# Kernel tuning notes

Measured on AMD Instinct MI355X. Metric: run time of the kernel, lower is better.

The kernel has to match this reference:

```python
import jax, jax.numpy as jnp
import numpy as np

HID = 256
OUT_DIM = 3


def _nearest_idx(c, size):
    # PyTorch grid_sample nearest, align_corners=False: idx = round(((c+1)*size-1)/2) = floor((c+1)*size/2)
    return jnp.clip(jnp.floor((c + 1.0) * size * 0.5), 0, size - 1).astype(jnp.int32)


def _mlp(x, params):
    # 4 hidden ReLU layers of 256 + linear out (LIIF imnet)
    for w, b in params[:-1]:
        x = jax.nn.relu(x @ w + b)
    w, b = params[-1]
    return x @ w + b


def setup_inputs() -> dict:
    key = jax.random.key(0)
    ks = jax.random.split(key, 16)
    B, C, H, W = 2, 64, 128, 128
    Q = 65536  # 256x256 HR queries
    feat = jax.random.normal(ks[0], (B, C, H, W), dtype=jnp.float32)
    coord = jax.random.uniform(ks[1], (B, Q, 2), dtype=jnp.float32) * 2.0 - 1.0  # in [-1,1)
    cell = jnp.full((B, Q, 2), 2.0 / 256.0, dtype=jnp.float32)
    in_dim = C * 9 + 2 + 2
    dims = [in_dim, HID, HID, HID, HID, OUT_DIM]
    inp = {"feat": feat, "coord": coord, "cell": cell}
    for i in range(5):
        fan_in = dims[i]
        inp[f"w{i}"] = jax.random.normal(ks[2 + 2 * i], (dims[i], dims[i + 1]), dtype=jnp.float32) / np.sqrt(fan_in)
        inp[f"b{i}"] = jnp.zeros((dims[i + 1],), dtype=jnp.float32)
    return inp


def reference(feat, coord, cell, w0, b0, w1, b1, w2, b2, w3, b3, w4, b4):
    params = [(w0, b0), (w1, b1), (w2, b2), (w3, b3), (w4, b4)]
    B, C, H, W = feat.shape
    dt = feat.dtype
    # feat_unfold: F.unfold(feat, 3, padding=1) -> channel order c*9 + (ki*3+kj)
    p = jnp.pad(feat, ((0, 0), (0, 0), (1, 1), (1, 1)))
    feat_u = jnp.stack([p[:, :, i:i + H, j:j + W] for i in range(3) for j in range(3)], axis=2)
    feat_flat = feat_u.reshape(B, C * 9, H * W)  # [B, 576, H*W]

    rx = 1.0 / H  # 2/H/2
    ry = 1.0 / W
    eps_shift = 1e-6
    lim = 1.0 - 1e-6
    rel_cell = cell * jnp.array([H, W], dtype=dt)

    preds, areas = [], []
    for vx in (-1.0, 1.0):
        for vy in (-1.0, 1.0):
            cx = jnp.clip(coord[..., 0] + vx * rx + eps_shift, -lim, lim)
            cy = jnp.clip(coord[..., 1] + vy * ry + eps_shift, -lim, lim)
            ix = _nearest_idx(cx, H)  # coord dim 0 -> height, grid is coord.flip(-1)
            iy = _nearest_idx(cy, W)
            lin = ix * W + iy  # [B, Q]
            q_feat = jnp.take_along_axis(feat_flat, lin[:, None, :], axis=2).transpose(0, 2, 1)  # [B,Q,576]
            # feat_coord grid-center values at the gathered cell (nearest gather of make_coord)
            qx = -1.0 + (2.0 * ix.astype(dt) + 1.0) / H
            qy = -1.0 + (2.0 * iy.astype(dt) + 1.0) / W
            rel = jnp.stack([(coord[..., 0] - qx) * H, (coord[..., 1] - qy) * W], axis=-1)  # [B,Q,2]
            mlp_in = jnp.concatenate([q_feat, rel, rel_cell], axis=-1)  # [B,Q,580]
            preds.append(_mlp(mlp_in, params))  # [B,Q,3]
            areas.append(jnp.abs(rel[..., 0] * rel[..., 1]) + 1e-9)

    # local_ensemble: swap diagonal areas
    areas[0], areas[3] = areas[3], areas[0]
    areas[1], areas[2] = areas[2], areas[1]
    tot = areas[0] + areas[1] + areas[2] + areas[3]
    ret = sum(pr * (a / tot)[..., None] for pr, a in zip(preds, areas))
    return ret
```

## Files before the change

### kernel.cpp

```cpp
#include <hip/hip_runtime.h>

typedef _Float16 half_t;
typedef _Float16 half4 __attribute__((ext_vector_type(4)));
typedef _Float16 half8 __attribute__((ext_vector_type(8)));
typedef float float4v __attribute__((ext_vector_type(4)));

#define MFMA16(a, b, c) __builtin_amdgcn_mfma_f32_16x16x32_f16(a, b, c, 0, 0, 0)

__device__ __host__ __forceinline__ int sigma_p(int s) {
  return (s & 0xC3) | ((s & 0x0C) << 2) | ((s & 0x30) >> 2);
}

__global__ __launch_bounds__(256) void pack_frags(
    const float* __restrict__ w0, const float* __restrict__ w1,
    const float* __restrict__ w2, const float* __restrict__ w3,
    const float* __restrict__ w4, half_t* __restrict__ w0p,
    half_t* __restrict__ w1p, half_t* __restrict__ w2p,
    half_t* __restrict__ w3p, half_t* __restrict__ w4p,
    half_t* __restrict__ wtp) {
  const int bb = blockIdx.x;
  const int tid = threadIdx.x;
  if (bb == 42) {
#pragma unroll
    for (int e = 0; e < 16; e++) {
      const int id = e * 256 + tid;
      const int j = id & 7;
      const int lane = (id >> 3) & 63;
      const int ks = id >> 9;
      const int n = lane & 15;
      const int k = ks * 32 + ((lane >> 4) << 3) + j;
      w4p[id] = (half_t)((n < 3) ? w4[sigma_p(k) * 3 + n] : 0.0f);
    }
#pragma unroll
    for (int e = 0; e < 4; e++)
      wtp[e * 256 + tid] = (half_t)w0[576 * 256 + e * 256 + sigma_p(tid)];
    return;
  }
  __shared__ float Wt[32][260];
  const float* w;
  half_t* out;
  int nks, ks;
  int mode;
  if (bb < 18) { w = w0; out = w0p; nks = 18; ks = bb; mode = 0; }
  else if (bb < 26) { w = w1; out = w1p; nks = 8; ks = bb - 18; mode = 1; }
  else if (bb < 34) { w = w2; out = w2p; nks = 8; ks = bb - 26; mode = 1; }
  else { w = w3; out = w3p; nks = 8; ks = bb - 34; mode = 1; }
  {
    const int n4 = (tid & 63) * 4;
    const int kr = tid >> 6;
#pragma unroll
    for (int e = 0; e < 8; e++) {
      const int kp = e * 4 + kr;
      int kg = ks * 32 + kp;
      if (mode == 0) { const int w9 = kg >> 6, c = kg & 63; kg = c * 9 + w9; }
      else kg = sigma_p(kg);
      *(float4v*)&Wt[kp][n4] = *(const float4v*)(w + (size_t)kg * 256 + n4);
    }
  }
  __syncthreads();
  const int lane = tid & 63;
  const int l15 = lane & 15;
  const int kq = (lane >> 4) << 3;
#pragma unroll
  for (int e = 0; e < 4; e++) {
    const int nt = e * 4 + (tid >> 6);
    half8 hv;
#pragma unroll
    for (int j = 0; j < 8; j++) hv[j] = (half_t)Wt[kq + j][nt * 16 + l15];
    *(half8*)&out[((nt * nks + ks) * 64 + lane) * 8] = hv;
  }
}

__global__ __launch_bounds__(256, 2) void conv_l0(
    const float* __restrict__ feat, const half_t* __restrict__ w0p,
    const float* __restrict__ b0, half_t* __restrict__ Z) {
  __shared__ alignas(16) half_t Xc[2][64][40];
  const int tid = threadIdx.x;
  const int lane = tid & 63, wave = tid >> 6, quad = lane >> 4, l15 = lane & 15;
  const int blk = blockIdx.x;
  const int b = blk >> 8;
  const int h = (blk >> 1) & 127;
  const int wbase = (blk & 1) << 6;
  const float* featB = feat + b * (64 * 128 * 128);

  auto stage = [&](int ks, int buf) {
    const int w9 = ks >> 1;
    const int di = w9 / 3;
    const int dj = w9 - 3 * di;
    const int pos = tid & 63;
    const int grp = tid >> 6;
    const int y = h + di - 1;
    const int x = wbase + pos + dj - 1;
    const bool ok = ((unsigned)y < 128u) && ((unsigned)x < 128u);
    const float* base = featB + (((ks & 1) * 32 + grp * 8) << 14) + (y << 7) + x;
    half4 h0, h1;
#pragma unroll
    for (int u = 0; u < 4; u++) h0[u] = (half_t)(ok ? base[u << 14] : 0.0f);
#pragma unroll
    for (int u = 0; u < 4; u++) h1[u] = (half_t)(ok ? base[(u + 4) << 14] : 0.0f);
    *(half4*)&Xc[buf][pos][grp * 8] = h0;
    *(half4*)&Xc[buf][pos][grp * 8 + 4] = h1;
  };

  const float4v zero4 = {0.0f, 0.0f, 0.0f, 0.0f};
  float4v acc[4][4];
#pragma unroll
  for (int mt = 0; mt < 4; mt++)
#pragma unroll
    for (int jn = 0; jn < 4; jn++) acc[mt][jn] = zero4;

  half8 bcur[4], bnxt[4];
#pragma unroll
  for (int jn = 0; jn < 4; jn++)
    bcur[jn] = *(const half8*)(w0p + ((((wave * 4 + jn) * 18 + 0) * 64 + lane) << 3));
  stage(0, 0);
  __syncthreads();

#pragma unroll 1
  for (int ks = 0; ks < 18; ks++) {
    const int buf = ks & 1;
    if (ks + 1 < 18) {
      stage(ks + 1, buf ^ 1);
#pragma unroll
      for (int jn = 0; jn < 4; jn++)
        bnxt[jn] =
            *(const half8*)(w0p + ((((wave * 4 + jn) * 18 + ks + 1) * 64 + lane) << 3));
    }
    half8 a[4];
#pragma unroll
    for (int mt = 0; mt < 4; mt++)
      a[mt] = *(const half8*)(&Xc[buf][mt * 16 + l15][quad * 8]);
#pragma unroll
    for (int mt = 0; mt < 4; mt++)
#pragma unroll
      for (int jn = 0; jn < 4; jn++)
        acc[mt][jn] = MFMA16(bcur[jn], a[mt], acc[mt][jn]);
#pragma unroll
    for (int jn = 0; jn < 4; jn++) bcur[jn] = bnxt[jn];
    __syncthreads();
  }

  float4v bb[4];
#pragma unroll
  for (int jn = 0; jn < 4; jn++)
    bb[jn] = *(const float4v*)(b0 + (wave * 4 + jn) * 16 + quad * 4);
  const int posbase = b * 16384 + h * 128 + wbase;
#pragma unroll
  for (int mt = 0; mt < 4; mt++) {
    half8 o0, o1;
#pragma unroll
    for (int jn = 0; jn < 2; jn++)
#pragma unroll
      for (int rr = 0; rr < 4; rr++) {
        o0[jn * 4 + rr] = (half_t)(acc[mt][jn][rr] + bb[jn][rr]);
        o1[jn * 4 + rr] = (half_t)(acc[mt][jn + 2][rr] + bb[jn + 2][rr]);
      }
    half_t* zp = &Z[(size_t)(posbase + mt * 16 + l15) * 256 + wave * 64 + quad * 16];
    *(half8*)zp = o0;
    *(half8*)(zp + 8) = o1;
  }
}

__global__ __launch_bounds__(256, 2) void liif_main(
    const float* __restrict__ coord, const float* __restrict__ cell,
    const half_t* __restrict__ Zp, const half_t* __restrict__ wtp,
    const half_t* __restrict__ w1p, const half_t* __restrict__ w2p,
    const half_t* __restrict__ w3p, const half_t* __restrict__ w4p,
    const float* __restrict__ b1, const float* __restrict__ b2,
    const float* __restrict__ b3, const float* __restrict__ b4,
    float* __restrict__ outp) {
  __shared__ alignas(16) half_t Hs[128][264];
  __shared__ float S4[4][128][4];
  __shared__ int pos4[4][64];
  __shared__ half_t relxh[4][64], relyh[4][64];
  __shared__ half_t cellxh[64], cellyh[64];
  __shared__ float area4[4][64];
  __shared__ float oacc[64][4];

  const int tid = threadIdx.x;
  const int lane = tid & 63;
  const int wave = tid >> 6;
  const int quad = lane >> 4;
  const int l15 = lane & 15;
  const int blk = blockIdx.x;
  const int batch = blk >> 10;

  {
    const int t = tid >> 6, row = tid & 63;
    const int gq = blk * 64 + row;
    const float cx0 = coord[gq * 2 + 0], cy0 = coord[gq * 2 + 1];
    const float vx = (t & 2) ? 1.0f : -1.0f;
    const float vy = (t & 1) ? 1.0f : -1.0f;
    const float r = 1.0f / 128.0f, lim = 1.0f - 1e-6f, eps = 1e-6f;
    float cx = fminf(fmaxf(cx0 + vx * r + eps, -lim), lim);
    float cy = fminf(fmaxf(cy0 + vy * r + eps, -lim), lim);
    int ix = (int)floorf((cx + 1.0f) * 64.0f);
    ix = min(max(ix, 0), 127);
    int iy = (int)floorf((cy + 1.0f) * 64.0f);
    iy = min(max(iy, 0), 127);
    float qx = -1.0f + (2.0f * ix + 1.0f) * (1.0f / 128.0f);
    float qy = -1.0f + (2.0f * iy + 1.0f) * (1.0f / 128.0f);
    float rxv = (cx0 - qx) * 128.0f;
    float ryv = (cy0 - qy) * 128.0f;
    pos4[t][row] = (batch << 14) + (ix << 7) + iy;
    relxh[t][row] = (half_t)rxv;
    relyh[t][row] = (half_t)ryv;
    area4[t][row] = fabsf(rxv * ryv) + 1e-9f;
    if (t == 0) {
      cellxh[row] = (half_t)(cell[gq * 2 + 0] * 128.0f);
      cellyh[row] = (half_t)(cell[gq * 2 + 1] * 128.0f);
      oacc[row][0] = 0.0f;
      oacc[row][1] = 0.0f;
      oacc[row][2] = 0.0f;
    }
  }
  __syncthreads();

  const float4v zero4 = {0.0f, 0.0f, 0.0f, 0.0f};
  const half8 zero8 = {0, 0, 0, 0, 0, 0, 0, 0};
  const int c8 = tid & 31;
  const int rbase = (tid >> 5) * 16;

  const half8 wt0 = *(const half8*)(wtp + 0 * 256 + c8 * 8);
  const half8 wt1 = *(const half8*)(wtp + 1 * 256 + c8 * 8);
  const half8 wt2 = *(const half8*)(wtp + 2 * 256 + c8 * 8);
  const half8 wt3 = *(const half8*)(wtp + 3 * 256 + c8 * 8);

  half8 bcur[4], bnxt[4], bf4[2];
#pragma unroll
  for (int jn = 0; jn < 4; jn++)
    bcur[jn] = *(const half8*)(w1p + ((((wave * 4 + jn) * 8 + 0) * 64 + lane) << 3));

#pragma unroll 1
  for (int p = 0; p < 2; p++) {
#pragma unroll
    for (int e = 0; e < 16; e++) {
      const int r = rbase + e;
      const int corner = 2 * p + (r >> 6);
      const int qrow = r & 63;
      const half8 z = *(const half8*)(Zp + ((size_t)pos4[corner][qrow] << 8) + c8 * 8);
      const half_t rx = relxh[corner][qrow], ry = relyh[corner][qrow];
      const half_t cx = cellxh[qrow], cy = cellyh[qrow];
      const half8 rx8 = {rx, rx, rx, rx, rx, rx, rx, rx};
      const half8 ry8 = {ry, ry, ry, ry, ry, ry, ry, ry};
      const half8 cx8 = {cx, cx, cx, cx, cx, cx, cx, cx};
      const half8 cy8 = {cy, cy, cy, cy, cy, cy, cy, cy};
      half8 v = z + rx8 * wt0 + ry8 * wt1 + cx8 * wt2 + cy8 * wt3;
      v = __builtin_elementwise_max(v, zero8);
      *(half8*)(&Hs[r][c8 * 8]) = v;
    }
    __syncthreads();

    float4v acc[8][4];
#pragma unroll 1
    for (int L = 0; L < 3; L++) {
      const half_t* wp = (L == 0) ? w1p : (L == 1) ? w2p : w3p;
      const float* bp = (L == 0) ? b1 : (L == 1) ? b2 : b3;
#pragma unroll
      for (int mt = 0; mt < 8; mt++)
#pragma unroll
        for (int jn = 0; jn < 4; jn++) acc[mt][jn] = zero4;
#pragma unroll 1
      for (int ks = 0; ks < 8; ks++) {
        if (ks + 1 < 8) {
#pragma unroll
          for (int jn = 0; jn < 4; jn++)
            bnxt[jn] =
                *(const half8*)(wp + ((((wave * 4 + jn) * 8 + ks + 1) * 64 + lane) << 3));
        }
        half8 a[8];
#pragma unroll
        for (int mt = 0; mt < 8; mt++)
          a[mt] = *(const half8*)(&Hs[mt * 16 + l15][ks * 32 + quad * 8]);
#pragma unroll
        for (int mt = 0; mt < 8; mt++)
#pragma unroll
          for (int jn = 0; jn < 4; jn++)
            acc[mt][jn] = MFMA16(bcur[jn], a[mt], acc[mt][jn]);
#pragma unroll
        for (int jn = 0; jn < 4; jn++) bcur[jn] = bnxt[jn];
      }
      __syncthreads();
      if (L < 2) {
        const half_t* wpn = (L == 0) ? w2p : w3p;
#pragma unroll
        for (int jn = 0; jn < 4; jn++)
          bcur[jn] = *(const half8*)(wpn + ((((wave * 4 + jn) * 8 + 0) * 64 + lane) << 3));
      } else {
#pragma unroll
        for (int kx = 0; kx < 2; kx++)
          bf4[kx] = *(const half8*)(w4p + (((wave * 2 + kx) * 64 + lane) << 3));
      }
      float4v bb[4];
#pragma unroll
      for (int jn = 0; jn < 4; jn++)
        bb[jn] = *(const float4v*)(bp + (wave * 4 + jn) * 16 + quad * 4);
#pragma unroll
      for (int mt = 0; mt < 8; mt++) {
        half8 o0, o1;
#pragma unroll
        for (int jn = 0; jn < 2; jn++)
#pragma unroll
          for (int rr = 0; rr < 4; rr++) {
            o0[jn * 4 + rr] = (half_t)fmaxf(acc[mt][jn][rr] + bb[jn][rr], 0.0f);
            o1[jn * 4 + rr] = (half_t)fmaxf(acc[mt][jn + 2][rr] + bb[jn + 2][rr], 0.0f);
          }
        half_t* hp = &Hs[mt * 16 + l15][wave * 64 + quad * 16];
        *(half8*)hp = o0;
        *(half8*)(hp + 8) = o1;
      }
      __syncthreads();
    }

    float4v acc4[8];
#pragma unroll
    for (int mt = 0; mt < 8; mt++) acc4[mt] = zero4;
#pragma unroll
    for (int kx = 0; kx < 2; kx++) {
      const int ks = wave * 2 + kx;
#pragma unroll
      for (int mt = 0; mt < 8; mt++) {
        half8 a = *(const half8*)(&Hs[mt * 16 + l15][ks * 32 + quad * 8]);
        acc4[mt] = MFMA16(a, bf4[kx], acc4[mt]);
      }
    }
    if (l15 < 4) {
#pragma unroll
      for (int mt = 0; mt < 8; mt++)
#pragma unroll
        for (int rr = 0; rr < 4; rr++)
          S4[wave][mt * 16 + quad * 4 + rr][l15] = acc4[mt][rr];
    }
    __syncthreads();

    if (p == 0) {
#pragma unroll
      for (int jn = 0; jn < 4; jn++)
        bcur[jn] = *(const half8*)(w1p + ((((wave * 4 + jn) * 8 + 0) * 64 + lane) << 3));
    }

    if (tid < 192) {
      const int qrow = tid / 3;
      const int j = tid - qrow * 3;
      const int ca = 2 * p, cb = 2 * p + 1;
      float pa = b4[j] + S4[0][qrow][j] + S4[1][qrow][j] + S4[2][qrow][j] + S4[3][qrow][j];
      float pb = b4[j] + S4[0][qrow + 64][j] + S4[1][qrow + 64][j] +
                 S4[2][qrow + 64][j] + S4[3][qrow + 64][j];
      oacc[qrow][j] += pa * area4[3 - ca][qrow] + pb * area4[3 - cb][qrow];
    }
    __syncthreads();
  }

  if (tid < 192) {
    const int qrow = tid / 3;
    const int j = tid - qrow * 3;
    const float tot =
        area4[0][qrow] + area4[1][qrow] + area4[2][qrow] + area4[3][qrow];
    outp[(blk * 64 + qrow) * 3 + j] = oacc[qrow][j] / tot;
  }
}

extern "C" void kernel_launch(void* const* d_in, const int* in_sizes, int n_in,
                              void* d_out, int out_size, void* d_ws, size_t ws_size,
                              hipStream_t stream) {
  const float* feat = (const float*)d_in[0];
  const float* coord = (const float*)d_in[1];
  const float* cell = (const float*)d_in[2];
  const float* w0 = (const float*)d_in[3];
  const float* b0 = (const float*)d_in[4];
  const float* w1 = (const float*)d_in[5];
  const float* b1 = (const float*)d_in[6];
  const float* w2 = (const float*)d_in[7];
  const float* b2 = (const float*)d_in[8];
  const float* w3 = (const float*)d_in[9];
  const float* b3 = (const float*)d_in[10];
  const float* w4 = (const float*)d_in[11];
  const float* b4 = (const float*)d_in[12];

  half_t* w0p = (half_t*)d_ws;
  half_t* w1p = w0p + 147456;
  half_t* w2p = w1p + 65536;
  half_t* w3p = w2p + 65536;
  half_t* w4p = w3p + 65536;
  half_t* wtp = w4p + 4096;
  half_t* Z = (half_t*)d_ws + 524288;

  pack_frags<<<43, 256, 0, stream>>>(w0, w1, w2, w3, w4, w0p, w1p, w2p, w3p, w4p, wtp);
  conv_l0<<<512, 256, 0, stream>>>(feat, w0p, b0, Z);
  liif_main<<<2048, 256, 0, stream>>>(coord, cell, Z, wtp, w1p, w2p, w3p, w4p, b1, b2,
                                      b3, b4, (float*)d_out);
}
```

Baseline: 326.4 us.

## Shrink conv_l0 tiles for more blocks and alias S4 onto Hs

conv_l0 now handles 32 positions per block instead of 64, launches twice as many blocks with launch bounds raised to 4 per CU, and drops the register double-buffering of weight fragments in favour of loading them at each step. The aim is more parallelism and occupancy in the conv stage. In liif_main the separate S4 reduction buffer is removed and its data is stored in the Hs tile, which gets a wider padded row (280) plus an extra barrier. This lowers LDS use and can change bank-conflict behaviour, at the cost of one more sync per pass and more redundant weight loads.

```diff
diff --git a/kernel.cpp b/kernel.cpp
--- a/kernel.cpp
+++ b/kernel.cpp
@@ -71,72 +71,64 @@
   }
 }
 
-__global__ __launch_bounds__(256, 2) void conv_l0(
+__global__ __launch_bounds__(256, 4) void conv_l0(
     const float* __restrict__ feat, const half_t* __restrict__ w0p,
     const float* __restrict__ b0, half_t* __restrict__ Z) {
-  __shared__ alignas(16) half_t Xc[2][64][40];
+  __shared__ alignas(16) half_t Xc[2][32][40];
   const int tid = threadIdx.x;
   const int lane = tid & 63, wave = tid >> 6, quad = lane >> 4, l15 = lane & 15;
   const int blk = blockIdx.x;
-  const int b = blk >> 8;
-  const int h = (blk >> 1) & 127;
-  const int wbase = (blk & 1) << 6;
+  const int b = blk >> 9;
+  const int h = (blk >> 2) & 127;
+  const int wbase = (blk & 3) << 5;
   const float* featB = feat + b * (64 * 128 * 128);
 
   auto stage = [&](int ks, int buf) {
     const int w9 = ks >> 1;
     const int di = w9 / 3;
     const int dj = w9 - 3 * di;
-    const int pos = tid & 63;
-    const int grp = tid >> 6;
+    const int pos = tid & 31;
+    const int grp = tid >> 5;
     const int y = h + di - 1;
     const int x = wbase + pos + dj - 1;
     const bool ok = ((unsigned)y < 128u) && ((unsigned)x < 128u);
-    const float* base = featB + (((ks & 1) * 32 + grp * 8) << 14) + (y << 7) + x;
-    half4 h0, h1;
-#pragma unroll
-    for (int u = 0; u < 4; u++) h0[u] = (half_t)(ok ? base[u << 14] : 0.0f);
-#pragma unroll
-    for (int u = 0; u < 4; u++) h1[u] = (half_t)(ok ? base[(u + 4) << 14] : 0.0f);
-    *(half4*)&Xc[buf][pos][grp * 8] = h0;
-    *(half4*)&Xc[buf][pos][grp * 8 + 4] = h1;
+    const float* base = featB + (((ks & 1) * 32 + grp * 4) << 14) + (y << 7) + x;
+    half4 hv;
+#pragma unroll
+    for (int u = 0; u < 4; u++) hv[u] = (half_t)(ok ? base[u << 14] : 0.0f);
+    *(half4*)&Xc[buf][pos][grp * 4] = hv;
   };
 
   const float4v zero4 = {0.0f, 0.0f, 0.0f, 0.0f};
-  float4v acc[4][4];
-#pragma unroll
-  for (int mt = 0; mt < 4; mt++)
+  float4v acc[2][4];
+#pragma unroll
+  for (int mt = 0; mt < 2; mt++)
 #pragma unroll
     for (int jn = 0; jn < 4; jn++) acc[mt][jn] = zero4;
 
-  half8 bcur[4], bnxt[4];
-#pragma unroll
-  for (int jn = 0; jn < 4; jn++)
-    bcur[jn] = *(const half8*)(w0p + ((((wave * 4 + jn) * 18 + 0) * 64 + lane) << 3));
   stage(0, 0);
   __syncthreads();
 
 #pragma unroll 1
   for (int ks = 0; ks < 18; ks++) {
     const int buf = ks & 1;
+    half8 bw[4];
+#pragma unroll
+    for (int jn = 0; jn < 4; jn++)
+      bw[jn] = *(const half8*)(w0p + ((((wave * 4 + jn) * 18 + ks) * 64 + lane) << 3));
+    half8 a[2];
+#pragma unroll
+    for (int mt = 0; mt < 2; mt++)
+      a[mt] = *(const half8*)(&Xc[buf][mt * 16 + l15][quad * 8]);
     if (ks + 1 < 18) {
+      __syncthreads();
       stage(ks + 1, buf ^ 1);
+    }
+#pragma unroll
+    for (int mt = 0; mt < 2; mt++)
 #pragma unroll
       for (int jn = 0; jn < 4; jn++)
-        bnxt[jn] =
-            *(const half8*)(w0p + ((((wave * 4 + jn) * 18 + ks + 1) * 64 + lane) << 3));
-    }
-    half8 a[4];
-#pragma unroll
-    for (int mt = 0; mt < 4; mt++)
-      a[mt] = *(const half8*)(&Xc[buf][mt * 16 + l15][quad * 8]);
-#pragma unroll
-    for (int mt = 0; mt < 4; mt++)
-#pragma unroll
-      for (int jn = 0; jn < 4; jn++)
-        acc[mt][jn] = MFMA16(bcur[jn], a[mt], acc[mt][jn]);
-#pragma unroll
-    for (int jn = 0; jn < 4; jn++) bcur[jn] = bnxt[jn];
+        acc[mt][jn] = MFMA16(bw[jn], a[mt], acc[mt][jn]);
     __syncthreads();
   }
 
@@ -146,7 +138,7 @@
     bb[jn] = *(const float4v*)(b0 + (wave * 4 + jn) * 16 + quad * 4);
   const int posbase = b * 16384 + h * 128 + wbase;
 #pragma unroll
-  for (int mt = 0; mt < 4; mt++) {
+  for (int mt = 0; mt < 2; mt++) {
     half8 o0, o1;
 #pragma unroll
     for (int jn = 0; jn < 2; jn++)
@@ -169,8 +161,7 @@
     const float* __restrict__ b1, const float* __restrict__ b2,
     const float* __restrict__ b3, const float* __restrict__ b4,
     float* __restrict__ outp) {
-  __shared__ alignas(16) half_t Hs[128][264];
-  __shared__ float S4[4][128][4];
+  __shared__ alignas(16) half_t Hs[128][280];
   __shared__ int pos4[4][64];
   __shared__ half_t relxh[4][64], relyh[4][64];
   __shared__ half_t cellxh[64], cellyh[64];
@@ -324,12 +315,14 @@
         acc4[mt] = MFMA16(a, bf4[kx], acc4[mt]);
       }
     }
+    __syncthreads();
+    float* S4f = (float*)&Hs[0][0];
     if (l15 < 4) {
 #pragma unroll
       for (int mt = 0; mt < 8; mt++)
 #pragma unroll
         for (int rr = 0; rr < 4; rr++)
-          S4[wave][mt * 16 + quad * 4 + rr][l15] = acc4[mt][rr];
+          S4f[((wave * 128 + mt * 16 + quad * 4 + rr) << 2) + l15] = acc4[mt][rr];
     }
     __syncthreads();
 
@@ -343,9 +336,13 @@
       const int qrow = tid / 3;
       const int j = tid - qrow * 3;
       const int ca = 2 * p, cb = 2 * p + 1;
-      float pa = b4[j] + S4[0][qrow][j] + S4[1][qrow][j] + S4[2][qrow][j] + S4[3][qrow][j];
-      float pb = b4[j] + S4[0][qrow + 64][j] + S4[1][qrow + 64][j] +
-                 S4[2][qrow + 64][j] + S4[3][qrow + 64][j];
+      float pa = b4[j] + S4f[((0 * 128 + qrow) << 2) + j] +
+                 S4f[((1 * 128 + qrow) << 2) + j] + S4f[((2 * 128 + qrow) << 2) + j] +
+                 S4f[((3 * 128 + qrow) << 2) + j];
+      float pb = b4[j] + S4f[((0 * 128 + 64 + qrow) << 2) + j] +
+                 S4f[((1 * 128 + 64 + qrow) << 2) + j] +
+                 S4f[((2 * 128 + 64 + qrow) << 2) + j] +
+                 S4f[((3 * 128 + 64 + qrow) << 2) + j];
       oacc[qrow][j] += pa * area4[3 - ca][qrow] + pb * area4[3 - cb][qrow];
     }
     __syncthreads();
@@ -386,7 +383,7 @@
   half_t* Z = (half_t*)d_ws + 524288;
 
   pack_frags<<<43, 256, 0, stream>>>(w0, w1, w2, w3, w4, w0p, w1p, w2p, w3p, w4p, wtp);
-  conv_l0<<<512, 256, 0, stream>>>(feat, w0p, b0, Z);
+  conv_l0<<<1024, 256, 0, stream>>>(feat, w0p, b0, Z);
   liif_main<<<2048, 256, 0, stream>>>(coord, cell, Z, wtp, w1p, w2p, w3p, w4p, b1, b2,
                                       b3, b4, (float*)d_out);
 }
```

After: 318.5 us. -2.4%, faster.
